# Performance work log

Hardware: AMD Instinct MI355X
Metric: run time of the kernel (lower is better)

## Reference

```python
import jax, jax.numpy as jnp
import numpy as np

NUM_HEADS = 8
QK_DIM = 64
V_DIM = 64


def _conv1x1(W, b, x):
    # W: [out, in], x: [N, in, T, V] -> [N, out, T, V]
    return jnp.einsum('oc,nctv->notv', W, x) + b[None, :, None, None]


def setup_inputs() -> dict:
    key = jax.random.key(0)
    ks = jax.random.split(key, 10)
    N, C, T, V = 8, 256, 1024, 25
    s = 0.02
    return {
        'feature': jax.random.normal(ks[0], (N, C, T, V), jnp.float32),
        'text_feature': jax.random.normal(ks[1], (1, 512, 1, V), jnp.float32),
        'Wq': jax.random.normal(ks[2], (NUM_HEADS * QK_DIM, 512), jnp.float32) * s,
        'bq': jax.random.normal(ks[3], (NUM_HEADS * QK_DIM,), jnp.float32) * s,
        'Wk': jax.random.normal(ks[4], (NUM_HEADS * QK_DIM, 512), jnp.float32) * s,
        'bk': jax.random.normal(ks[5], (NUM_HEADS * QK_DIM,), jnp.float32) * s,
        'Wv': jax.random.normal(ks[6], (V_DIM, C), jnp.float32) * s,
        'bv': jax.random.normal(ks[7], (V_DIM,), jnp.float32) * s,
        'Wo': jax.random.normal(ks[8], (C, NUM_HEADS * V_DIM), jnp.float32) * s,
        'bo': jax.random.normal(ks[9], (C,), jnp.float32) * s,
    }


def reference(feature, text_feature, Wq, bq, Wk, bk, Wv, bv, Wo, bo):
    N, C, T, V = feature.shape
    tf = jnp.broadcast_to(text_feature, (N, 512, 1, V))  # expand over batch
    # Q/K from text features (T dim collapses to 1)
    q = _conv1x1(Wq, bq, tf).reshape(N, NUM_HEADS, QK_DIM, V)
    k = _conv1x1(Wk, bk, tf).reshape(N, NUM_HEADS, QK_DIM, V)
    v = _conv1x1(Wv, bv, feature)  # [N, v_dim, T, V]
    energy = jnp.einsum('nhcu,nhcv->nhuv', q, k) / jnp.sqrt(jnp.float32(QK_DIM))
    attn = jax.nn.softmax(energy, axis=-1)  # [N, H, V, V]
    z = jnp.einsum('nctu,nhuv->nhctv', v, attn).reshape(N, NUM_HEADS * V_DIM, T, V)
    out = _conv1x1(Wo, bo, z) + feature
    return out
```

## Files before the change

### kernel.cpp

```cpp
#include <hip/hip_runtime.h>
#include <hip/hip_bf16.h>


typedef __attribute__((ext_vector_type(8))) short short8;
typedef __attribute__((ext_vector_type(4))) short short4v;
typedef __attribute__((ext_vector_type(4))) float f4v;

static __device__ __forceinline__ unsigned short f2bf(float f) {
  union { float f; unsigned u; } v; v.f = f;
  unsigned r = v.u + 0x7fffu + ((v.u >> 16) & 1u);
  return (unsigned short)(r >> 16);
}
static __device__ __forceinline__ float bf2f(unsigned short h) {
  union { unsigned u; float f; } v; v.u = ((unsigned)h) << 16;
  return v.f;
}


__global__ void k_qk_conv(const float* __restrict__ tf,
                          const float* __restrict__ Wq, const float* __restrict__ bq,
                          const float* __restrict__ Wk, const float* __restrict__ bk,
                          const float* __restrict__ Wv, const float* __restrict__ Wo,
                          unsigned short* __restrict__ WvP,
                          unsigned short* __restrict__ WoP,
                          float* __restrict__ qkP)
{
  __shared__ float tfl[12800];
  const int b = blockIdx.x, tid = threadIdx.x;
  if (b < 100) {
    for (int i = tid; i < 12800; i += 256) tfl[i] = tf[i];
    __syncthreads();
    int idx = b * 256 + tid;
    int isK = idx >= 12800;
    int j = isK ? idx - 12800 : idx;
    int g = j / 25, u = j - 25 * g;
    const float* wrow = (isK ? Wk : Wq) + g * 512;
    float s = (isK ? bk : bq)[g];
    for (int i = 0; i < 512; ++i) s += wrow[i] * tfl[i * 25 + u];
    qkP[idx] = s;
  } else {
    int cb = b - 100;
    for (int i = cb * 256 + tid; i < 16384; i += 64 * 256) {
      WvP[i] = f2bf(Wv[i]);
    }
    for (int i = cb * 256 + tid; i < 131072; i += 64 * 256) {
      int hh = i >> 14, rr = i & 16383;
      int o = rr >> 6, kk = rr & 63;
      WoP[i] = f2bf(Wo[o * 512 + hh * 64 + kk]);
    }
  }
}

__global__ void k_attn(const float* __restrict__ qkP,
                       unsigned short* __restrict__ attnP)
{
  __shared__ float ql[1600], kl[1600], attl[625];
  const int h = blockIdx.x, tid = threadIdx.x;
  for (int i = tid; i < 1600; i += 256) {
    ql[i] = qkP[h * 1600 + i];
    kl[i] = qkP[12800 + h * 1600 + i];
  }
  __syncthreads();
  if (tid < 25) {
    int u = tid;
    float e[25];
    float mx = -1e30f;
    #pragma unroll
    for (int v = 0; v < 25; ++v) {
      float s = 0.f;
      #pragma unroll
      for (int r = 0; r < 64; ++r) s += ql[r * 25 + u] * kl[r * 25 + v];
      s *= 0.125f;
      e[v] = s;
      mx = fmaxf(mx, s);
    }
    float den = 0.f;
    #pragma unroll
    for (int v = 0; v < 25; ++v) { e[v] = __expf(e[v] - mx); den += e[v]; }
    float inv = 1.f / den;
    #pragma unroll
    for (int v = 0; v < 25; ++v) attl[u * 25 + v] = e[v] * inv;
  }
  __syncthreads();
  for (int i = tid; i < 1280; i += 256) {
    int vp = i / 40, u = i - 40 * vp;
    attnP[h * 1280 + i] =
        (vp < 25 && u < 25) ? f2bf(attl[u * 25 + vp]) : (unsigned short)0;
  }
}

__launch_bounds__(512, 6)
__global__ void k_main(const float* __restrict__ feature,
                       const float* __restrict__ bv,
                       const float* __restrict__ bo,
                       const unsigned short* __restrict__ WvP,
                       const unsigned short* __restrict__ WoP,
                       const unsigned short* __restrict__ attnP,
                       float* __restrict__ out)
{
  extern __shared__ char smem[];
  unsigned short* Fl = (unsigned short*)smem;
  unsigned short* Vl = (unsigned short*)(smem + 33792);
  unsigned short* Zl = (unsigned short*)(smem + 43008);

  const int tid  = threadIdx.x;
  const int wave = tid >> 6;
  const int lane = tid & 63;
  const int quad = lane >> 4;
  const int l16  = lane & 15;
  const int n  = blockIdx.x >> 9;
  const int tb = blockIdx.x & 511;
  const int t0 = tb * 2;

  {
    short8 z = {0, 0, 0, 0, 0, 0, 0, 0};
    short8* fz = (short8*)smem;
    for (int i = tid; i < 2112; i += 512) fz[i] = z;
  }
  __syncthreads();

  {
    const int c = tid >> 1, p = tid & 1;
    const float2* src = reinterpret_cast<const float2*>(
        feature + ((size_t)(n * 256 + c) * 1024 + t0) * 25);
    for (int i = p; i < 25; i += 2) {
      float2 f = src[i];
      int j0 = 2 * i;
      {
        int j = j0;       int t = (j >= 25); int vp = j - 25 * t;
        Fl[(t * 32 + vp) * 264 + c] = f2bf(f.x);
      }
      {
        int j = j0 + 1;   int t = (j >= 25); int vp = j - 25 * t;
        Fl[(t * 32 + vp) * 264 + c] = f2bf(f.y);
      }
    }
  }
  __syncthreads();

  f4v acc[2][4];
  #pragma unroll
  for (int mi = 0; mi < 2; ++mi) {
    #pragma unroll
    for (int r = 0; r < 4; ++r) {
      int o = wave * 32 + mi * 16 + quad * 4 + r;
      float bor = bo[o];
      #pragma unroll
      for (int ni = 0; ni < 4; ++ni) {
        int colb = ni * 16 + l16;
        acc[mi][ni][r] = bor + bf2f(Fl[colb * 264 + o]);
      }
    }
  }

  {
    const int mt1 = wave & 3, nh1 = wave >> 2;
    f4v accv[2];
    #pragma unroll
    for (int ni = 0; ni < 2; ++ni) {
      #pragma unroll
      for (int r = 0; r < 4; ++r) accv[ni][r] = bv[mt1 * 16 + quad * 4 + r];
    }
    #pragma unroll
    for (int ks = 0; ks < 8; ++ks) {
      short8 a = *reinterpret_cast<const short8*>(
          WvP + (mt1 * 16 + l16) * 256 + ks * 32 + quad * 8);
      #pragma unroll
      for (int ni = 0; ni < 2; ++ni) {
        int colb = (2 * nh1 + ni) * 16 + l16;
        short8 b = *reinterpret_cast<const short8*>(
            &Fl[colb * 264 + ks * 32 + quad * 8]);
        accv[ni] = __builtin_amdgcn_mfma_f32_16x16x32_bf16(a, b, accv[ni], 0, 0, 0);
      }
    }
    #pragma unroll
    for (int ni = 0; ni < 2; ++ni) {
      int colb = (2 * nh1 + ni) * 16 + l16;
      #pragma unroll
      for (int r = 0; r < 4; ++r) {
        int c = mt1 * 16 + quad * 4 + r;
        Vl[c * 72 + colb] = f2bf(accv[ni][r]);
      }
    }
  }
  __syncthreads();

  #pragma unroll 1
  for (int h = 0; h < 8; ++h) {
    {
      const int am = wave >> 1;
      const int np = wave & 1;
      short8 a = *reinterpret_cast<const short8*>(
          &Vl[(am * 16 + l16) * 72 + np * 32 + quad * 8]);
      f4v accz[2];
      #pragma unroll
      for (int j = 0; j < 2; ++j) {
        f4v z = {0.f, 0.f, 0.f, 0.f};
        short8 b = *reinterpret_cast<const short8*>(
            attnP + h * 1280 + (j * 16 + l16) * 40 + quad * 8);
        accz[j] = __builtin_amdgcn_mfma_f32_16x16x32_bf16(a, b, z, 0, 0, 0);
      }
      #pragma unroll
      for (int j = 0; j < 2; ++j) {
        int col = np * 32 + j * 16 + l16;
        int c0 = am * 16 + quad * 4;
        short4v zz;
        #pragma unroll
        for (int r = 0; r < 4; ++r) zz[r] = (short)f2bf(accz[j][r]);
        *reinterpret_cast<short4v*>(&Zl[col * 72 + c0]) = zz;
      }
    }
    __syncthreads();

    {
      const unsigned short* __restrict__ woh = WoP + h * 16384;
      #pragma unroll
      for (int ks = 0; ks < 2; ++ks) {
        short8 bfr[4], afr[2];
        #pragma unroll
        for (int ni = 0; ni < 4; ++ni)
          bfr[ni] = *reinterpret_cast<const short8*>(
              &Zl[(ni * 16 + l16) * 72 + ks * 32 + quad * 8]);
        #pragma unroll
        for (int mi = 0; mi < 2; ++mi)
          afr[mi] = *reinterpret_cast<const short8*>(
              woh + (wave * 32 + mi * 16 + l16) * 64 + ks * 32 + quad * 8);
        #pragma unroll
        for (int mi = 0; mi < 2; ++mi) {
          #pragma unroll
          for (int ni = 0; ni < 4; ++ni)
            acc[mi][ni] =
                __builtin_amdgcn_mfma_f32_16x16x32_bf16(afr[mi], bfr[ni], acc[mi][ni], 0, 0, 0);
        }
      }
    }
    __syncthreads();
  }

  #pragma unroll
  for (int ni = 0; ni < 4; ++ni) {
    int colb = ni * 16 + l16;
    int t = colb >> 5, vp = colb & 31;
    if (vp < 25) {
      #pragma unroll
      for (int mi = 0; mi < 2; ++mi) {
        #pragma unroll
        for (int r = 0; r < 4; ++r) {
          int o = wave * 32 + mi * 16 + quad * 4 + r;
          out[((size_t)(n * 256 + o) * 1024 + (t0 + t)) * 25 + vp] = acc[mi][ni][r];
        }
      }
    }
  }
}

extern "C" void kernel_launch(void* const* d_in, const int* in_sizes, int n_in,
                              void* d_out, int out_size, void* d_ws, size_t ws_size,
                              hipStream_t stream)
{
  const float* feature = (const float*)d_in[0];
  const float* tf      = (const float*)d_in[1];
  const float* Wq      = (const float*)d_in[2];
  const float* bq      = (const float*)d_in[3];
  const float* Wk      = (const float*)d_in[4];
  const float* bk      = (const float*)d_in[5];
  const float* Wv      = (const float*)d_in[6];
  const float* bv      = (const float*)d_in[7];
  const float* Wo      = (const float*)d_in[8];
  const float* bo      = (const float*)d_in[9];
  float* out = (float*)d_out;

  unsigned short* WvP   = (unsigned short*)d_ws;
  unsigned short* WoP   = WvP + 16384;
  unsigned short* attnP = WoP + 131072;
  float* qkP = (float*)(attnP + 10240);

  hipLaunchKernelGGL(k_qk_conv, dim3(164), dim3(256), 0, stream,
                     tf, Wq, bq, Wk, bk, Wv, Wo, WvP, WoP, qkP);
  hipLaunchKernelGGL(k_attn, dim3(8), dim3(256), 0, stream, qkP, attnP);

  hipLaunchKernelGGL(k_main, dim3(4096), dim3(512), 52224, stream,
                     feature, bv, bo, WvP, WoP, attnP, out);
}
```

Before: 593.8 us.

## Compute all heads' Z at once and run a single K=512 output GEMM

```diff
diff --git a/kernel.cpp b/kernel.cpp
--- a/kernel.cpp
+++ b/kernel.cpp
@@ -44,9 +44,7 @@
       WvP[i] = f2bf(Wv[i]);
     }
     for (int i = cb * 256 + tid; i < 131072; i += 64 * 256) {
-      int hh = i >> 14, rr = i & 16383;
-      int o = rr >> 6, kk = rr & 63;
-      WoP[i] = f2bf(Wo[o * 512 + hh * 64 + kk]);
+      WoP[i] = f2bf(Wo[i]);
     }
   }
 }
@@ -89,7 +87,7 @@
   }
 }
 
-__launch_bounds__(512, 6)
+__launch_bounds__(512, 4)
 __global__ void k_main(const float* __restrict__ feature,
                        const float* __restrict__ bv,
                        const float* __restrict__ bo,
@@ -100,24 +98,24 @@
 {
   extern __shared__ char smem[];
   unsigned short* Fl = (unsigned short*)smem;
-  unsigned short* Vl = (unsigned short*)(smem + 33792);
-  unsigned short* Zl = (unsigned short*)(smem + 43008);
+  unsigned short* Zl = (unsigned short*)smem;
+  unsigned short* Vl = (unsigned short*)(smem + 66560);
 
   const int tid  = threadIdx.x;
   const int wave = tid >> 6;
   const int lane = tid & 63;
   const int quad = lane >> 4;
   const int l16  = lane & 15;
-  const int n  = blockIdx.x >> 9;
-  const int tb = blockIdx.x & 511;
+  const int n  = blockIdx.x & 7;
+  const int tb = blockIdx.x >> 3;
   const int t0 = tb * 2;
 
-  {
+  if (tid < 462) {
     short8 z = {0, 0, 0, 0, 0, 0, 0, 0};
-    short8* fz = (short8*)smem;
-    for (int i = tid; i < 2112; i += 512) fz[i] = z;
-  }
-  __syncthreads();
+    int pc = tid / 33, off = tid - 33 * pc;
+    int t = pc / 7, vp = 25 + (pc - 7 * t);
+    *reinterpret_cast<short8*>(&Fl[(t * 32 + vp) * 264 + off * 8]) = z;
+  }
 
   {
     const int c = tid >> 1, p = tid & 1;
@@ -136,25 +134,34 @@
       }
     }
   }
+
+  const int mt1 = wave & 3, nh1 = wave >> 2;
+  short8 wa[8];
+  #pragma unroll
+  for (int ks = 0; ks < 8; ++ks)
+    wa[ks] = *reinterpret_cast<const short8*>(
+        WvP + (mt1 * 16 + l16) * 256 + ks * 32 + quad * 8);
+
   __syncthreads();
 
   f4v acc[2][4];
   #pragma unroll
   for (int mi = 0; mi < 2; ++mi) {
-    #pragma unroll
-    for (int r = 0; r < 4; ++r) {
-      int o = wave * 32 + mi * 16 + quad * 4 + r;
-      float bor = bo[o];
-      #pragma unroll
-      for (int ni = 0; ni < 4; ++ni) {
-        int colb = ni * 16 + l16;
-        acc[mi][ni][r] = bor + bf2f(Fl[colb * 264 + o]);
-      }
+    const int o0 = wave * 32 + mi * 16 + quad * 4;
+    float bo4[4];
+    #pragma unroll
+    for (int r = 0; r < 4; ++r) bo4[r] = bo[o0 + r];
+    #pragma unroll
+    for (int ni = 0; ni < 4; ++ni) {
+      short4v fr = *reinterpret_cast<const short4v*>(
+          &Fl[(ni * 16 + l16) * 264 + o0]);
+      #pragma unroll
+      for (int r = 0; r < 4; ++r)
+        acc[mi][ni][r] = bo4[r] + bf2f((unsigned short)fr[r]);
     }
   }
 
   {
-    const int mt1 = wave & 3, nh1 = wave >> 2;
     f4v accv[2];
     #pragma unroll
     for (int ni = 0; ni < 2; ++ni) {
@@ -163,14 +170,12 @@
     }
     #pragma unroll
     for (int ks = 0; ks < 8; ++ks) {
-      short8 a = *reinterpret_cast<const short8*>(
-          WvP + (mt1 * 16 + l16) * 256 + ks * 32 + quad * 8);
       #pragma unroll
       for (int ni = 0; ni < 2; ++ni) {
         int colb = (2 * nh1 + ni) * 16 + l16;
         short8 b = *reinterpret_cast<const short8*>(
             &Fl[colb * 264 + ks * 32 + quad * 8]);
-        accv[ni] = __builtin_amdgcn_mfma_f32_16x16x32_bf16(a, b, accv[ni], 0, 0, 0);
+        accv[ni] = __builtin_amdgcn_mfma_f32_16x16x32_bf16(wa[ks], b, accv[ni], 0, 0, 0);
       }
     }
     #pragma unroll
@@ -183,58 +188,69 @@
       }
     }
   }
-  __syncthreads();
-
-  #pragma unroll 1
-  for (int h = 0; h < 8; ++h) {
-    {
-      const int am = wave >> 1;
-      const int np = wave & 1;
-      short8 a = *reinterpret_cast<const short8*>(
-          &Vl[(am * 16 + l16) * 72 + np * 32 + quad * 8]);
-      f4v accz[2];
-      #pragma unroll
-      for (int j = 0; j < 2; ++j) {
-        f4v z = {0.f, 0.f, 0.f, 0.f};
-        short8 b = *reinterpret_cast<const short8*>(
-            attnP + h * 1280 + (j * 16 + l16) * 40 + quad * 8);
-        accz[j] = __builtin_amdgcn_mfma_f32_16x16x32_bf16(a, b, z, 0, 0, 0);
-      }
-      #pragma unroll
-      for (int j = 0; j < 2; ++j) {
-        int col = np * 32 + j * 16 + l16;
-        int c0 = am * 16 + quad * 4;
-        short4v zz;
-        #pragma unroll
-        for (int r = 0; r < 4; ++r) zz[r] = (short)f2bf(accz[j][r]);
-        *reinterpret_cast<short4v*>(&Zl[col * 72 + c0]) = zz;
-      }
-    }
-    __syncthreads();
-
-    {
-      const unsigned short* __restrict__ woh = WoP + h * 16384;
-      #pragma unroll
-      for (int ks = 0; ks < 2; ++ks) {
-        short8 bfr[4], afr[2];
-        #pragma unroll
-        for (int ni = 0; ni < 4; ++ni)
-          bfr[ni] = *reinterpret_cast<const short8*>(
-              &Zl[(ni * 16 + l16) * 72 + ks * 32 + quad * 8]);
-        #pragma unroll
-        for (int mi = 0; mi < 2; ++mi)
-          afr[mi] = *reinterpret_cast<const short8*>(
-              woh + (wave * 32 + mi * 16 + l16) * 64 + ks * 32 + quad * 8);
-        #pragma unroll
-        for (int mi = 0; mi < 2; ++mi) {
-          #pragma unroll
-          for (int ni = 0; ni < 4; ++ni)
-            acc[mi][ni] =
-                __builtin_amdgcn_mfma_f32_16x16x32_bf16(afr[mi], bfr[ni], acc[mi][ni], 0, 0, 0);
-        }
-      }
-    }
-    __syncthreads();
+
+  const int t2 = wave >> 2, q2 = wave & 3;
+  short8 ab[4];
+  #pragma unroll
+  for (int nj = 0; nj < 4; ++nj) {
+    int h = 2 * q2 + (nj >> 1), vph = nj & 1;
+    ab[nj] = *reinterpret_cast<const short8*>(
+        attnP + h * 1280 + (vph * 16 + l16) * 40 + quad * 8);
+  }
+
+  __syncthreads();
+
+  #pragma unroll
+  for (int mi = 0; mi < 4; ++mi) {
+    short8 a = *reinterpret_cast<const short8*>(
+        &Vl[(mi * 16 + l16) * 72 + t2 * 32 + quad * 8]);
+    #pragma unroll
+    for (int nj = 0; nj < 4; ++nj) {
+      f4v z = {0.f, 0.f, 0.f, 0.f};
+      f4v accz = __builtin_amdgcn_mfma_f32_16x16x32_bf16(a, ab[nj], z, 0, 0, 0);
+      int h = 2 * q2 + (nj >> 1), vph = nj & 1;
+      int col = t2 * 32 + vph * 16 + l16;
+      int k0 = h * 64 + mi * 16 + quad * 4;
+      short4v zz;
+      #pragma unroll
+      for (int r = 0; r < 4; ++r) zz[r] = (short)f2bf(accz[r]);
+      *reinterpret_cast<short4v*>(&Zl[col * 520 + k0]) = zz;
+    }
+  }
+
+  short8 af01[2][2];
+  #pragma unroll
+  for (int pk = 0; pk < 2; ++pk)
+    #pragma unroll
+    for (int mi = 0; mi < 2; ++mi)
+      af01[pk][mi] = *reinterpret_cast<const short8*>(
+          WoP + (wave * 32 + mi * 16 + l16) * 512 + pk * 32 + quad * 8);
+
+  __syncthreads();
+
+  #pragma unroll
+  for (int ks = 0; ks < 16; ++ks) {
+    short8 bfr[4], afr[2];
+    #pragma unroll
+    for (int ni = 0; ni < 4; ++ni)
+      bfr[ni] = *reinterpret_cast<const short8*>(
+          &Zl[(ni * 16 + l16) * 520 + ks * 32 + quad * 8]);
+    if (ks < 2) {
+      afr[0] = af01[ks][0];
+      afr[1] = af01[ks][1];
+    } else {
+      #pragma unroll
+      for (int mi = 0; mi < 2; ++mi)
+        afr[mi] = *reinterpret_cast<const short8*>(
+            WoP + (wave * 32 + mi * 16 + l16) * 512 + ks * 32 + quad * 8);
+    }
+    #pragma unroll
+    for (int mi = 0; mi < 2; ++mi) {
+      #pragma unroll
+      for (int ni = 0; ni < 4; ++ni)
+        acc[mi][ni] =
+            __builtin_amdgcn_mfma_f32_16x16x32_bf16(afr[mi], bfr[ni], acc[mi][ni], 0, 0, 0);
+    }
   }
 
   #pragma unroll
@@ -279,6 +295,8 @@
                      tf, Wq, bq, Wk, bk, Wv, Wo, WvP, WoP, qkP);
   hipLaunchKernelGGL(k_attn, dim3(8), dim3(256), 0, stream, qkP, attnP);
 
-  hipLaunchKernelGGL(k_main, dim3(4096), dim3(512), 52224, stream,
+  hipFuncSetAttribute(reinterpret_cast<const void*>(&k_main),
+                      hipFuncAttributeMaxDynamicSharedMemorySize, 75776);
+  hipLaunchKernelGGL(k_main, dim3(4096), dim3(512), 75776, stream,
                      feature, bv, bo, WvP, WoP, attnP, out);
 }
```

Measured after the change: 547.7 us. -7.8%, faster.
